# Kernel tuning notes

Hardware: AMD Instinct MI355X
Metric: run time of the kernel (lower is better)

Reference implementation:

```python
import jax, jax.numpy as jnp
import numpy as np

N_NODES = 100000
N_EDGES = 1600000
N_GRAPHS = 1024
D_IN = 128
D_HID = 128
D_OUT = 2


def setup_inputs() -> dict:
    key = jax.random.key(0)
    ks = jax.random.split(key, 12)
    x = jax.random.normal(ks[0], (N_NODES, D_IN), dtype=jnp.float32)
    edge_index = jax.random.randint(ks[1], (2, N_EDGES), 0, N_NODES, dtype=jnp.int32)
    batch = jnp.sort(jax.random.randint(ks[2], (N_NODES,), 0, N_GRAPHS, dtype=jnp.int32))
    def lin(k, fan_in, fan_out):
        bound = 1.0 / np.sqrt(fan_in)
        kw, kb = jax.random.split(k)
        W = jax.random.uniform(kw, (fan_in, fan_out), minval=-bound, maxval=bound, dtype=jnp.float32)
        b = jax.random.uniform(kb, (fan_out,), minval=-bound, maxval=bound, dtype=jnp.float32)
        return W, b
    W1, b1 = lin(ks[3], D_IN, D_HID)
    W2, b2 = lin(ks[4], D_HID, D_HID)
    fc1_w, fc1_b = lin(ks[5], D_HID, D_HID)
    fc2_w, fc2_b = lin(ks[6], D_HID, D_OUT)
    return {"x": x, "edge_index": edge_index, "batch": batch,
            "W1": W1, "b1": b1, "W2": W2, "b2": b2,
            "fc1_w": fc1_w, "fc1_b": fc1_b, "fc2_w": fc2_w, "fc2_b": fc2_b}


def gcn_conv(x, W, b, src, dst, deg_inv_sqrt, n_nodes):
    # GCNConv: out = D^-1/2 (A + I) D^-1/2 (x W) + b, using edge list with self-loops
    h = x @ W  # [N, d_out]
    norm = deg_inv_sqrt[src] * deg_inv_sqrt[dst]  # [E+N]
    msg = h[src] * norm[:, None]  # gather + scale
    out = jnp.zeros((n_nodes, h.shape[1]), dtype=h.dtype).at[dst].add(msg)
    return out + b


def reference(x, edge_index, batch, W1, b1, W2, b2, fc1_w, fc1_b, fc2_w, fc2_b):
    n = x.shape[0]
    loops = jnp.arange(n, dtype=edge_index.dtype)
    src = jnp.concatenate([edge_index[0], loops])  # add self-loops (PyG default)
    dst = jnp.concatenate([edge_index[1], loops])
    deg = jnp.zeros((n,), dtype=x.dtype).at[dst].add(1.0)
    deg_inv_sqrt = jax.lax.rsqrt(deg)  # deg >= 1 due to self-loops

    h = jax.nn.relu(gcn_conv(x, W1, b1, src, dst, deg_inv_sqrt, n))
    # dropout p=0.5 is identity in eval mode
    h = jax.nn.relu(gcn_conv(h, W2, b2, src, dst, deg_inv_sqrt, n))

    # global_mean_pool over batch assignment
    sums = jax.ops.segment_sum(h, batch, num_segments=N_GRAPHS)
    cnts = jax.ops.segment_sum(jnp.ones((n,), dtype=h.dtype), batch, num_segments=N_GRAPHS)
    pooled = sums / jnp.maximum(cnts, 1.0)[:, None]  # [G, d]

    g = jax.nn.relu(pooled @ fc1_w + fc1_b)
    logits = g @ fc2_w + fc2_b
    return jax.nn.log_softmax(logits, axis=1)
```

## Files before the change

### kernel.cpp

```cpp
#include <hip/hip_runtime.h>
#include <hip/hip_fp16.h>
#include <math.h>


#define D_FEAT 128
#define BSHIFT 9
#define BNODES 512
#define CHUNK 4096
#define CAPB 16384
#define PCAP 16384
#define CAP 10240

using half8   = __attribute__((ext_vector_type(8))) _Float16;
using half4   = __attribute__((ext_vector_type(4))) _Float16;
using floatx4 = __attribute__((ext_vector_type(4))) float;
using floatx2 = __attribute__((ext_vector_type(2))) float;

__global__ void __launch_bounds__(256) binA_kernel(const int* __restrict__ edges,
                                                   int* __restrict__ gcur,
                                                   int* __restrict__ binned, int E, int nb) {
    __shared__ int h[256];
    __shared__ int cur[256];
    __shared__ int base[256];
    int t = threadIdx.x;
    int c0 = blockIdx.x * CHUNK;
    int sv[CHUNK / 256], bv[CHUNK / 256];
    int i0 = c0 + t * (CHUNK / 256);
    if (i0 + (CHUNK / 256) <= E) {
#pragma unroll
        for (int k = 0; k < CHUNK / 256; k += 4) {
            int4 s4 = *(const int4*)&edges[i0 + k];
            int4 d4 = *(const int4*)&edges[E + i0 + k];
            bv[k + 0] = d4.x >> BSHIFT; sv[k + 0] = ((d4.x & (BNODES - 1)) << 17) | s4.x;
            bv[k + 1] = d4.y >> BSHIFT; sv[k + 1] = ((d4.y & (BNODES - 1)) << 17) | s4.y;
            bv[k + 2] = d4.z >> BSHIFT; sv[k + 2] = ((d4.z & (BNODES - 1)) << 17) | s4.z;
            bv[k + 3] = d4.w >> BSHIFT; sv[k + 3] = ((d4.w & (BNODES - 1)) << 17) | s4.w;
        }
    } else {
#pragma unroll
        for (int k = 0; k < CHUNK / 256; ++k) {
            int i = i0 + k;
            if (i < E) {
                int s = edges[i], d = edges[E + i];
                bv[k] = d >> BSHIFT;
                sv[k] = ((d & (BNODES - 1)) << 17) | s;
            } else bv[k] = -1;
        }
    }
    h[t] = 0;
    __syncthreads();
#pragma unroll
    for (int k = 0; k < CHUNK / 256; ++k)
        if (bv[k] >= 0) atomicAdd(&h[bv[k]], 1);
    __syncthreads();
    if (t < nb && h[t] > 0) base[t] = atomicAdd(&gcur[t], h[t]);
    cur[t] = 0;
    __syncthreads();
#pragma unroll
    for (int k = 0; k < CHUNK / 256; ++k)
        if (bv[k] >= 0) {
            int b = bv[k];
            int r = atomicAdd(&cur[b], 1);
            int pos = base[b] + r;
            if (pos < CAPB) binned[b * CAPB + pos] = sv[k];
        }
}

__global__ void __launch_bounds__(256) binB_kernel(const int* __restrict__ binned,
                                                   const int* __restrict__ gcur,
                                                   float* __restrict__ dis,
                                                   int* __restrict__ rowbeg,
                                                   int* __restrict__ rowend,
                                                   int* __restrict__ csr,
                                                   int N, int nb) {
    __shared__ int hist[BNODES];
    __shared__ int cur[BNODES];
    __shared__ int pend[BNODES];
    __shared__ int sdata[256];
    __shared__ int vals[CAP];
    int t = threadIdx.x;
    int b = blockIdx.x;
    int node0 = b << BSHIFT;
    int cnt = gcur[b];
    const int* bin = binned + (size_t)b * CAPB;
    hist[t] = 0; hist[t + 256] = 0;
    __syncthreads();
    for (int i = t; i < cnt; i += 256) {
        int v = bin[i];
        if (i < CAP) vals[i] = v;
        atomicAdd(&hist[v >> 17], 1);
    }
    __syncthreads();
    int a0 = hist[2 * t], a1 = hist[2 * t + 1];
    int p0sz = (a0 + 15) & ~15, p1sz = (a1 + 15) & ~15;
    int pair = p0sz + p1sz;
    sdata[t] = pair;
    __syncthreads();
    for (int d = 1; d < 256; d <<= 1) {
        int u = (t >= d) ? sdata[t - d] : 0;
        __syncthreads();
        sdata[t] += u;
        __syncthreads();
    }
    int excl = sdata[t] - pair;
    int q0 = b * PCAP + excl, q1 = q0 + p0sz;
    cur[2 * t] = q0;
    cur[2 * t + 1] = q1;
    pend[2 * t] = q1;
    pend[2 * t + 1] = q1 + p1sz;
    int n0 = node0 + 2 * t, n1 = node0 + 2 * t + 1;
    if (n0 < N) {
        rowbeg[n0] = q0; rowend[n0] = q1;
        dis[n0] = rsqrtf((float)a0 + 1.0f);
    }
    if (n1 < N) {
        rowbeg[n1] = q1; rowend[n1] = q1 + p1sz;
        dis[n1] = rsqrtf((float)a1 + 1.0f);
    }
    __syncthreads();
    for (int i = t; i < cnt; i += 256) {
        int v = (i < CAP) ? vals[i] : bin[i];
        int p = atomicAdd(&cur[v >> 17], 1);
        csr[p] = v & 0x1FFFF;
    }
    __syncthreads();
    for (int i = t; i < BNODES; i += 256) {
        int e = pend[i];
        for (int p = cur[i]; p < e; ++p) csr[p] = N;
    }
}

__global__ void wprep_kernel(const float* __restrict__ W1, const float* __restrict__ W2,
                             _Float16* __restrict__ Wt1, _Float16* __restrict__ Wt2,
                             unsigned int* __restrict__ zrow) {
    int i = blockIdx.x * blockDim.x + threadIdx.x;
    int n = i >> 7, k = i & 127;
    Wt1[i] = (_Float16)W1[k * 128 + n];
    Wt2[i] = (_Float16)W2[k * 128 + n];
    if (i < 32) zrow[i] = 0u;
}

template <bool HALF_IN>
__global__ void __launch_bounds__(256) gemm_mfma_kernel(const void* __restrict__ Xv,
                                                        const _Float16* __restrict__ WtG,
                                                        const float* __restrict__ dis,
                                                        unsigned char* __restrict__ Y8, int N) {
    __shared__ _Float16 wt[128][136];
    int t = threadIdx.x;
    int row0 = blockIdx.x * 64;

#pragma unroll
    for (int i = 0; i < 8; ++i) {
        int c = t + i * 256;
        int r = c >> 4, c8 = (c & 15) * 8;
        *(half8*)&wt[r][c8] = *(const half8*)&WtG[r * 128 + c8];
    }

    int wave = t >> 6, lane = t & 63;
    int m = lane & 15, quad = lane >> 4;
    int grow = row0 + wave * 16 + m;

    half8 a[4];
    if (grow < N) {
        if (HALF_IN) {
            const _Float16* Xp = (const _Float16*)Xv;
#pragma unroll
            for (int k = 0; k < 4; ++k)
                a[k] = *(const half8*)&Xp[(size_t)grow * 128 + k * 32 + quad * 8];
        } else {
            const float* Xp = (const float*)Xv;
#pragma unroll
            for (int k = 0; k < 4; ++k) {
                float4 v0 = *(const float4*)&Xp[(size_t)grow * 128 + k * 32 + quad * 8];
                float4 v1 = *(const float4*)&Xp[(size_t)grow * 128 + k * 32 + quad * 8 + 4];
                a[k] = (half8){(_Float16)v0.x, (_Float16)v0.y, (_Float16)v0.z, (_Float16)v0.w,
                               (_Float16)v1.x, (_Float16)v1.y, (_Float16)v1.z, (_Float16)v1.w};
            }
        }
    } else {
#pragma unroll
        for (int k = 0; k < 4; ++k) a[k] = (half8){};
    }
    __syncthreads();

    floatx4 acc[8];
#pragma unroll
    for (int nt = 0; nt < 8; ++nt) acc[nt] = (floatx4){0.f, 0.f, 0.f, 0.f};
#pragma unroll
    for (int nt = 0; nt < 8; ++nt) {
#pragma unroll
        for (int k = 0; k < 4; ++k) {
            half8 bfr = *(const half8*)&wt[nt * 16 + m][k * 32 + quad * 8];
            acc[nt] = __builtin_amdgcn_mfma_f32_16x16x32_f16(a[k], bfr, acc[nt], 0, 0, 0);
        }
    }
    int orow = row0 + wave * 16 + quad * 4;
#pragma unroll
    for (int r = 0; r < 4; ++r) {
        int row = orow + r;
        if (row < N) {
            float dr = dis[row];
#pragma unroll
            for (int nt = 0; nt < 8; ++nt) {
                float v = acc[nt][r] * dr;
                unsigned char q =
                    (unsigned char)(__builtin_amdgcn_cvt_pk_fp8_f32(v, v, 0, false) & 0xff);
                Y8[(size_t)row * 128 + nt * 16 + m] = q;
            }
        }
    }
}

__global__ void __launch_bounds__(256) agg_kernel(const unsigned char* __restrict__ H8,
                                                  const int* __restrict__ rowbeg,
                                                  const int* __restrict__ rowend,
                                                  const int* __restrict__ csr,
                                                  const float* __restrict__ dis,
                                                  const float* __restrict__ bias,
                                                  _Float16* __restrict__ out, int N) {
    int v = (blockIdx.x * blockDim.x + threadIdx.x) >> 6;
    int lane = threadIdx.x & 63;
    if (v >= N) return;
    int half = lane >> 5, sl = lane & 31;
    int r0 = rowbeg[v], r1 = rowend[v];
    float dv = dis[v];
    unsigned fo = (unsigned)(sl << 2);

    floatx2 a01, a23;
    {
        unsigned int u = *(const unsigned int*)(H8 + (((unsigned)v << 7) | fo));
        floatx2 lo = __builtin_amdgcn_cvt_pk_f32_fp8(u, false);
        floatx2 hi = __builtin_amdgcn_cvt_pk_f32_fp8(u, true);
        floatx2 hf = {0.5f, 0.5f};
        a01 = hf * lo;
        a23 = hf * hi;
    }
#define ACC(uu)                                                         \
        {                                                               \
            a01 += __builtin_amdgcn_cvt_pk_f32_fp8(uu, false);          \
            a23 += __builtin_amdgcn_cvt_pk_f32_fp8(uu, true);           \
        }
    for (int e = r0 + half; e + 14 < r1; e += 16) {
        int s0 = csr[e],      s1 = csr[e + 2],  s2 = csr[e + 4],  s3 = csr[e + 6];
        int s4 = csr[e + 8],  s5 = csr[e + 10], s6 = csr[e + 12], s7 = csr[e + 14];
        unsigned int u0 = *(const unsigned int*)(H8 + (((unsigned)s0 << 7) | fo));
        unsigned int u1 = *(const unsigned int*)(H8 + (((unsigned)s1 << 7) | fo));
        unsigned int u2 = *(const unsigned int*)(H8 + (((unsigned)s2 << 7) | fo));
        unsigned int u3 = *(const unsigned int*)(H8 + (((unsigned)s3 << 7) | fo));
        unsigned int u4 = *(const unsigned int*)(H8 + (((unsigned)s4 << 7) | fo));
        unsigned int u5 = *(const unsigned int*)(H8 + (((unsigned)s5 << 7) | fo));
        unsigned int u6 = *(const unsigned int*)(H8 + (((unsigned)s6 << 7) | fo));
        unsigned int u7 = *(const unsigned int*)(H8 + (((unsigned)s7 << 7) | fo));
        ACC(u0) ACC(u1) ACC(u2) ACC(u3) ACC(u4) ACC(u5) ACC(u6) ACC(u7)
    }
#undef ACC
    a01[0] += __shfl_xor(a01[0], 32, 64);
    a01[1] += __shfl_xor(a01[1], 32, 64);
    a23[0] += __shfl_xor(a23[0], 32, 64);
    a23[1] += __shfl_xor(a23[1], 32, 64);
    if (half == 0) {
        float4 b = *(const float4*)&bias[sl * 4];
        half4 o = {(_Float16)fmaxf(dv * a01[0] + b.x, 0.f),
                   (_Float16)fmaxf(dv * a01[1] + b.y, 0.f),
                   (_Float16)fmaxf(dv * a23[0] + b.z, 0.f),
                   (_Float16)fmaxf(dv * a23[1] + b.w, 0.f)};
        *(half4*)&out[(size_t)v * 128 + sl * 4] = o;
    }
}

__device__ __forceinline__ int lower_bound_i(const int* a, int n, int key) {
    int lo = 0, hi = n;
    while (lo < hi) {
        int mid = (lo + hi) >> 1;
        if (a[mid] < key) lo = mid + 1;
        else hi = mid;
    }
    return lo;
}

__global__ void __launch_bounds__(512) poolhead_kernel(const _Float16* __restrict__ H,
                                                       const int* __restrict__ batch,
                                                       const float* __restrict__ fc1w,
                                                       const float* __restrict__ fc1b,
                                                       const float* __restrict__ fc2w,
                                                       const float* __restrict__ fc2b,
                                                       float* __restrict__ out, int N) {
    __shared__ int range[2];
    __shared__ float part[4][128];
    __shared__ float p[128];
    __shared__ float r0s[128], r1s[128];
    int g = blockIdx.x;
    int t = threadIdx.x;
    int j = t & 127, rg = t >> 7;
    if (t < 2) range[t] = lower_bound_i(batch, N, g + t);
    __syncthreads();
    int lo = range[0], hi = range[1];
    float s = 0.f;
    for (int v = lo + rg; v < hi; v += 4) s += (float)H[(size_t)v * 128 + j];
    part[rg][j] = s;
    __syncthreads();
    if (rg == 0) {
        float tot = part[0][j] + part[1][j] + part[2][j] + part[3][j];
        p[j] = tot / fmaxf((float)(hi - lo), 1.0f);
    }
    __syncthreads();
    if (t < 128) {
        float acc = fc1b[t];
#pragma unroll 8
        for (int k = 0; k < 128; ++k) acc = fmaf(p[k], fc1w[k * 128 + t], acc);
        float gv = fmaxf(acc, 0.f);
        r0s[t] = gv * fc2w[t * 2 + 0];
        r1s[t] = gv * fc2w[t * 2 + 1];
    }
    __syncthreads();
    for (int st = 64; st > 0; st >>= 1) {
        if (t < st) {
            r0s[t] += r0s[t + st];
            r1s[t] += r1s[t + st];
        }
        __syncthreads();
    }
    if (t == 0) {
        float l0 = r0s[0] + fc2b[0];
        float l1 = r1s[0] + fc2b[1];
        float m = fmaxf(l0, l1);
        float lse = m + logf(expf(l0 - m) + expf(l1 - m));
        out[g * 2 + 0] = l0 - lse;
        out[g * 2 + 1] = l1 - lse;
    }
}

extern "C" void kernel_launch(void* const* d_in, const int* in_sizes, int n_in,
                              void* d_out, int out_size, void* d_ws, size_t ws_size,
                              hipStream_t stream) {
    const float* x    = (const float*)d_in[0];
    const int* edges  = (const int*)d_in[1];
    const int* batch  = (const int*)d_in[2];
    const float* W1   = (const float*)d_in[3];
    const float* b1   = (const float*)d_in[4];
    const float* W2   = (const float*)d_in[5];
    const float* b2   = (const float*)d_in[6];
    const float* fc1w = (const float*)d_in[7];
    const float* fc1b = (const float*)d_in[8];
    const float* fc2w = (const float*)d_in[9];
    const float* fc2b = (const float*)d_in[10];
    float* out = (float*)d_out;

    int N = in_sizes[2];
    int E = in_sizes[1] / 2;
    int G = out_size / 2;
    int nb = (N + BNODES - 1) / BNODES;
    int nA = (E + CHUNK - 1) / CHUNK;

    char* ws = (char*)d_ws;
    size_t off = 0;
    auto alloc = [&](size_t bytes) -> char* {
        char* ptr = ws + off;
        off += (bytes + 255) & ~(size_t)255;
        return ptr;
    };
    int* gcur          = (int*)alloc((size_t)nb * 4);
    int* binned        = (int*)alloc((size_t)nb * CAPB * 4);
    int* rowbeg        = (int*)alloc((size_t)N * 4);
    int* rowend        = (int*)alloc((size_t)N * 4);
    float* dis         = (float*)alloc((size_t)N * 4);
    int* csr           = (int*)alloc((size_t)nb * PCAP * 4);
    _Float16* Wt1      = (_Float16*)alloc(128 * 128 * 2);
    _Float16* Wt2      = (_Float16*)alloc(128 * 128 * 2);
    unsigned char* buf8 = (unsigned char*)alloc((size_t)(N + 1) * D_FEAT);
    _Float16* bufH     = (_Float16*)alloc((size_t)N * D_FEAT * 2);

    hipMemsetAsync(gcur, 0, (size_t)nb * 4, stream);

    binA_kernel<<<nA, 256, 0, stream>>>(edges, gcur, binned, E, nb);
    binB_kernel<<<nb, 256, 0, stream>>>(binned, gcur, dis, rowbeg, rowend, csr, N, nb);
    wprep_kernel<<<64, 256, 0, stream>>>(W1, W2, Wt1, Wt2,
                                         (unsigned int*)(buf8 + (size_t)N * D_FEAT));

    int gAgg = (N * 64 + 255) / 256;
    int gGemm = (N + 63) / 64;
    gemm_mfma_kernel<false><<<gGemm, 256, 0, stream>>>((const void*)x, Wt1, dis, buf8, N);
    agg_kernel<<<gAgg, 256, 0, stream>>>(buf8, rowbeg, rowend, csr, dis, b1, bufH, N);
    gemm_mfma_kernel<true><<<gGemm, 256, 0, stream>>>((const void*)bufH, Wt2, dis, buf8, N);
    agg_kernel<<<gAgg, 256, 0, stream>>>(buf8, rowbeg, rowend, csr, dis, b2, bufH, N);
    poolhead_kernel<<<G, 512, 0, stream>>>(bufH, batch, fc1w, fc1b, fc2w, fc2b, out, N);
}
```

Before: 266.7 us.

## Fuse layer-1 aggregation with layer-2 GEMM into a single kernel

Replaces the first aggregation kernel plus the second GEMM with one kernel. Each block aggregates 16 nodes into an fp16 shared-memory tile, then runs MFMA against Wt2 and writes the dis-scaled fp8 output to a second buffer. This removes the fp16 round trip of the hidden features through global memory and one kernel launch. In exchange, each wave reads its Wt2 slice from global memory instead of shared memory, and the edge loop only handles full groups of 16 edges (rows are padded with zero-row indices).

```diff
diff --git a/kernel.cpp b/kernel.cpp
--- a/kernel.cpp
+++ b/kernel.cpp
@@ -132,12 +132,13 @@
 
 __global__ void wprep_kernel(const float* __restrict__ W1, const float* __restrict__ W2,
                              _Float16* __restrict__ Wt1, _Float16* __restrict__ Wt2,
-                             unsigned int* __restrict__ zrow) {
+                             unsigned int* __restrict__ zrow,
+                             unsigned int* __restrict__ zrow2) {
     int i = blockIdx.x * blockDim.x + threadIdx.x;
     int n = i >> 7, k = i & 127;
     Wt1[i] = (_Float16)W1[k * 128 + n];
     Wt2[i] = (_Float16)W2[k * 128 + n];
-    if (i < 32) zrow[i] = 0u;
+    if (i < 32) { zrow[i] = 0u; zrow2[i] = 0u; }
 }
 
 template <bool HALF_IN>
@@ -206,6 +207,104 @@
                 unsigned char q =
                     (unsigned char)(__builtin_amdgcn_cvt_pk_fp8_f32(v, v, 0, false) & 0xff);
                 Y8[(size_t)row * 128 + nt * 16 + m] = q;
+            }
+        }
+    }
+}
+
+__global__ void __launch_bounds__(256) fusedA_kernel(const unsigned char* __restrict__ H8,
+                                                     const int* __restrict__ rowbeg,
+                                                     const int* __restrict__ rowend,
+                                                     const int* __restrict__ csr,
+                                                     const float* __restrict__ dis,
+                                                     const float* __restrict__ bias,
+                                                     const _Float16* __restrict__ Wt2,
+                                                     unsigned char* __restrict__ Y8, int N) {
+    __shared__ _Float16 hl[16][136];
+    int t = threadIdx.x;
+    int wave = t >> 6, lane = t & 63;
+    int half = lane >> 5, sl = lane & 31;
+    unsigned fo = (unsigned)(sl << 2);
+    int vbase = blockIdx.x * 16 + wave * 4;
+
+#pragma unroll
+    for (int i = 0; i < 4; ++i) {
+        int v = vbase + i;
+        floatx2 a01 = {0.f, 0.f}, a23 = {0.f, 0.f};
+        float dv = 0.f;
+        if (v < N) {
+            int r0 = rowbeg[v], r1 = rowend[v];
+            dv = dis[v];
+            {
+                unsigned int u = *(const unsigned int*)(H8 + (((unsigned)v << 7) | fo));
+                floatx2 lo = __builtin_amdgcn_cvt_pk_f32_fp8(u, false);
+                floatx2 hi = __builtin_amdgcn_cvt_pk_f32_fp8(u, true);
+                floatx2 hf = {0.5f, 0.5f};
+                a01 = hf * lo;
+                a23 = hf * hi;
+            }
+#define ACC(uu)                                                         \
+            {                                                           \
+                a01 += __builtin_amdgcn_cvt_pk_f32_fp8(uu, false);      \
+                a23 += __builtin_amdgcn_cvt_pk_f32_fp8(uu, true);       \
+            }
+            for (int e = r0 + half; e + 14 < r1; e += 16) {
+                int s0 = csr[e],      s1 = csr[e + 2],  s2 = csr[e + 4],  s3 = csr[e + 6];
+                int s4 = csr[e + 8],  s5 = csr[e + 10], s6 = csr[e + 12], s7 = csr[e + 14];
+                unsigned int u0 = *(const unsigned int*)(H8 + (((unsigned)s0 << 7) | fo));
+                unsigned int u1 = *(const unsigned int*)(H8 + (((unsigned)s1 << 7) | fo));
+                unsigned int u2 = *(const unsigned int*)(H8 + (((unsigned)s2 << 7) | fo));
+                unsigned int u3 = *(const unsigned int*)(H8 + (((unsigned)s3 << 7) | fo));
+                unsigned int u4 = *(const unsigned int*)(H8 + (((unsigned)s4 << 7) | fo));
+                unsigned int u5 = *(const unsigned int*)(H8 + (((unsigned)s5 << 7) | fo));
+                unsigned int u6 = *(const unsigned int*)(H8 + (((unsigned)s6 << 7) | fo));
+                unsigned int u7 = *(const unsigned int*)(H8 + (((unsigned)s7 << 7) | fo));
+                ACC(u0) ACC(u1) ACC(u2) ACC(u3) ACC(u4) ACC(u5) ACC(u6) ACC(u7)
+            }
+#undef ACC
+        }
+        a01[0] += __shfl_xor(a01[0], 32, 64);
+        a01[1] += __shfl_xor(a01[1], 32, 64);
+        a23[0] += __shfl_xor(a23[0], 32, 64);
+        a23[1] += __shfl_xor(a23[1], 32, 64);
+        if (half == 0) {
+            float4 b = *(const float4*)&bias[sl * 4];
+            half4 o = {(_Float16)fmaxf(dv * a01[0] + b.x, 0.f),
+                       (_Float16)fmaxf(dv * a01[1] + b.y, 0.f),
+                       (_Float16)fmaxf(dv * a23[0] + b.z, 0.f),
+                       (_Float16)fmaxf(dv * a23[1] + b.w, 0.f)};
+            *(half4*)&hl[wave * 4 + i][sl * 4] = o;
+        }
+    }
+    __syncthreads();
+
+    int m = lane & 15, quad = lane >> 4;
+    half8 a[4];
+#pragma unroll
+    for (int k = 0; k < 4; ++k) a[k] = *(const half8*)&hl[m][k * 32 + quad * 8];
+    floatx4 acc[2];
+    acc[0] = (floatx4){0.f, 0.f, 0.f, 0.f};
+    acc[1] = (floatx4){0.f, 0.f, 0.f, 0.f};
+    int nt0 = wave * 2;
+#pragma unroll
+    for (int j = 0; j < 2; ++j)
+#pragma unroll
+        for (int k = 0; k < 4; ++k) {
+            half8 bfr = *(const half8*)&Wt2[(size_t)((nt0 + j) * 16 + m) * 128 + k * 32 + quad * 8];
+            acc[j] = __builtin_amdgcn_mfma_f32_16x16x32_f16(a[k], bfr, acc[j], 0, 0, 0);
+        }
+    int orow = blockIdx.x * 16 + quad * 4;
+#pragma unroll
+    for (int r = 0; r < 4; ++r) {
+        int row = orow + r;
+        if (row < N) {
+            float dr = dis[row];
+#pragma unroll
+            for (int j = 0; j < 2; ++j) {
+                float vv = acc[j][r] * dr;
+                unsigned char q =
+                    (unsigned char)(__builtin_amdgcn_cvt_pk_fp8_f32(vv, vv, 0, false) & 0xff);
+                Y8[(size_t)row * 128 + (nt0 + j) * 16 + m] = q;
             }
         }
     }
@@ -367,7 +466,8 @@
     int* csr           = (int*)alloc((size_t)nb * PCAP * 4);
     _Float16* Wt1      = (_Float16*)alloc(128 * 128 * 2);
     _Float16* Wt2      = (_Float16*)alloc(128 * 128 * 2);
-    unsigned char* buf8 = (unsigned char*)alloc((size_t)(N + 1) * D_FEAT);
+    unsigned char* buf8  = (unsigned char*)alloc((size_t)(N + 1) * D_FEAT);
+    unsigned char* buf8b = (unsigned char*)alloc((size_t)(N + 1) * D_FEAT);
     _Float16* bufH     = (_Float16*)alloc((size_t)N * D_FEAT * 2);
 
     hipMemsetAsync(gcur, 0, (size_t)nb * 4, stream);
@@ -375,13 +475,15 @@
     binA_kernel<<<nA, 256, 0, stream>>>(edges, gcur, binned, E, nb);
     binB_kernel<<<nb, 256, 0, stream>>>(binned, gcur, dis, rowbeg, rowend, csr, N, nb);
     wprep_kernel<<<64, 256, 0, stream>>>(W1, W2, Wt1, Wt2,
-                                         (unsigned int*)(buf8 + (size_t)N * D_FEAT));
+                                         (unsigned int*)(buf8 + (size_t)N * D_FEAT),
+                                         (unsigned int*)(buf8b + (size_t)N * D_FEAT));
 
     int gAgg = (N * 64 + 255) / 256;
     int gGemm = (N + 63) / 64;
+    int gFused = (N + 15) / 16;
     gemm_mfma_kernel<false><<<gGemm, 256, 0, stream>>>((const void*)x, Wt1, dis, buf8, N);
-    agg_kernel<<<gAgg, 256, 0, stream>>>(buf8, rowbeg, rowend, csr, dis, b1, bufH, N);
-    gemm_mfma_kernel<true><<<gGemm, 256, 0, stream>>>((const void*)bufH, Wt2, dis, buf8, N);
-    agg_kernel<<<gAgg, 256, 0, stream>>>(buf8, rowbeg, rowend, csr, dis, b2, bufH, N);
+    fusedA_kernel<<<gFused, 256, 0, stream>>>(buf8, rowbeg, rowend, csr, dis, b1, Wt2,
+                                              buf8b, N);
+    agg_kernel<<<gAgg, 256, 0, stream>>>(buf8b, rowbeg, rowend, csr, dis, b2, bufH, N);
     poolhead_kernel<<<G, 512, 0, stream>>>(bufH, batch, fc1w, fc1b, fc2w, fc2b, out, N);
 }
```

Measured after the change: 277.3 us. 4.0% more time.

## Build CSR with global atomic degree count, scan and scatter

Applied to the files above, without the earlier changes.

Replaces the two-stage binned CSR build with three kernels. The old scheme did a shared-memory histogram plus a bin append, then a per-bin local sort. The new scheme counts per-node degrees with global atomics, computes padded row offsets per 512-node block, and scatters source indices into CSR slots through global atomic cursors. It drops the large intermediate binned buffer and its extra read/write pass, but it reads the edge list twice and relies on many contended, scattered global atomics and uncoalesced writes.

```diff
diff --git a/kernel.cpp b/kernel.cpp
--- a/kernel.cpp
+++ b/kernel.cpp
@@ -6,92 +6,40 @@
 #define D_FEAT 128
 #define BSHIFT 9
 #define BNODES 512
-#define CHUNK 4096
-#define CAPB 16384
 #define PCAP 16384
-#define CAP 10240
 
 using half8   = __attribute__((ext_vector_type(8))) _Float16;
 using half4   = __attribute__((ext_vector_type(4))) _Float16;
 using floatx4 = __attribute__((ext_vector_type(4))) float;
 using floatx2 = __attribute__((ext_vector_type(2))) float;
 
-__global__ void __launch_bounds__(256) binA_kernel(const int* __restrict__ edges,
-                                                   int* __restrict__ gcur,
-                                                   int* __restrict__ binned, int E, int nb) {
-    __shared__ int h[256];
-    __shared__ int cur[256];
-    __shared__ int base[256];
-    int t = threadIdx.x;
-    int c0 = blockIdx.x * CHUNK;
-    int sv[CHUNK / 256], bv[CHUNK / 256];
-    int i0 = c0 + t * (CHUNK / 256);
-    if (i0 + (CHUNK / 256) <= E) {
-#pragma unroll
-        for (int k = 0; k < CHUNK / 256; k += 4) {
-            int4 s4 = *(const int4*)&edges[i0 + k];
-            int4 d4 = *(const int4*)&edges[E + i0 + k];
-            bv[k + 0] = d4.x >> BSHIFT; sv[k + 0] = ((d4.x & (BNODES - 1)) << 17) | s4.x;
-            bv[k + 1] = d4.y >> BSHIFT; sv[k + 1] = ((d4.y & (BNODES - 1)) << 17) | s4.y;
-            bv[k + 2] = d4.z >> BSHIFT; sv[k + 2] = ((d4.z & (BNODES - 1)) << 17) | s4.z;
-            bv[k + 3] = d4.w >> BSHIFT; sv[k + 3] = ((d4.w & (BNODES - 1)) << 17) | s4.w;
-        }
+__global__ void __launch_bounds__(256) deg_kernel(const int* __restrict__ edges,
+                                                  int* __restrict__ deg, int E) {
+    int i = (blockIdx.x * 256 + threadIdx.x) * 4;
+    if (i + 3 < E) {
+        int4 d4 = *(const int4*)&edges[E + i];
+        atomicAdd(&deg[d4.x], 1);
+        atomicAdd(&deg[d4.y], 1);
+        atomicAdd(&deg[d4.z], 1);
+        atomicAdd(&deg[d4.w], 1);
     } else {
-#pragma unroll
-        for (int k = 0; k < CHUNK / 256; ++k) {
-            int i = i0 + k;
-            if (i < E) {
-                int s = edges[i], d = edges[E + i];
-                bv[k] = d >> BSHIFT;
-                sv[k] = ((d & (BNODES - 1)) << 17) | s;
-            } else bv[k] = -1;
-        }
-    }
-    h[t] = 0;
-    __syncthreads();
-#pragma unroll
-    for (int k = 0; k < CHUNK / 256; ++k)
-        if (bv[k] >= 0) atomicAdd(&h[bv[k]], 1);
-    __syncthreads();
-    if (t < nb && h[t] > 0) base[t] = atomicAdd(&gcur[t], h[t]);
-    cur[t] = 0;
-    __syncthreads();
-#pragma unroll
-    for (int k = 0; k < CHUNK / 256; ++k)
-        if (bv[k] >= 0) {
-            int b = bv[k];
-            int r = atomicAdd(&cur[b], 1);
-            int pos = base[b] + r;
-            if (pos < CAPB) binned[b * CAPB + pos] = sv[k];
-        }
-}
-
-__global__ void __launch_bounds__(256) binB_kernel(const int* __restrict__ binned,
-                                                   const int* __restrict__ gcur,
+        for (; i < E; ++i) atomicAdd(&deg[edges[E + i]], 1);
+    }
+}
+
+__global__ void __launch_bounds__(256) scan_kernel(const int* __restrict__ deg,
                                                    float* __restrict__ dis,
                                                    int* __restrict__ rowbeg,
                                                    int* __restrict__ rowend,
-                                                   int* __restrict__ csr,
-                                                   int N, int nb) {
-    __shared__ int hist[BNODES];
-    __shared__ int cur[BNODES];
-    __shared__ int pend[BNODES];
+                                                   int* __restrict__ cur,
+                                                   int* __restrict__ csr, int N) {
     __shared__ int sdata[256];
-    __shared__ int vals[CAP];
     int t = threadIdx.x;
     int b = blockIdx.x;
     int node0 = b << BSHIFT;
-    int cnt = gcur[b];
-    const int* bin = binned + (size_t)b * CAPB;
-    hist[t] = 0; hist[t + 256] = 0;
-    __syncthreads();
-    for (int i = t; i < cnt; i += 256) {
-        int v = bin[i];
-        if (i < CAP) vals[i] = v;
-        atomicAdd(&hist[v >> 17], 1);
-    }
-    __syncthreads();
-    int a0 = hist[2 * t], a1 = hist[2 * t + 1];
+    int n0 = node0 + 2 * t, n1 = node0 + 2 * t + 1;
+    int a0 = (n0 < N) ? deg[n0] : 0;
+    int a1 = (n1 < N) ? deg[n1] : 0;
     int p0sz = (a0 + 15) & ~15, p1sz = (a1 + 15) & ~15;
     int pair = p0sz + p1sz;
     sdata[t] = pair;
@@ -104,29 +52,31 @@
     }
     int excl = sdata[t] - pair;
     int q0 = b * PCAP + excl, q1 = q0 + p0sz;
-    cur[2 * t] = q0;
-    cur[2 * t + 1] = q1;
-    pend[2 * t] = q1;
-    pend[2 * t + 1] = q1 + p1sz;
-    int n0 = node0 + 2 * t, n1 = node0 + 2 * t + 1;
     if (n0 < N) {
-        rowbeg[n0] = q0; rowend[n0] = q1;
+        rowbeg[n0] = q0; rowend[n0] = q1; cur[n0] = q0;
         dis[n0] = rsqrtf((float)a0 + 1.0f);
+        for (int p = q0 + a0; p < q1; ++p) csr[p] = N;
     }
     if (n1 < N) {
-        rowbeg[n1] = q1; rowend[n1] = q1 + p1sz;
+        rowbeg[n1] = q1; rowend[n1] = q1 + p1sz; cur[n1] = q1;
         dis[n1] = rsqrtf((float)a1 + 1.0f);
-    }
-    __syncthreads();
-    for (int i = t; i < cnt; i += 256) {
-        int v = (i < CAP) ? vals[i] : bin[i];
-        int p = atomicAdd(&cur[v >> 17], 1);
-        csr[p] = v & 0x1FFFF;
-    }
-    __syncthreads();
-    for (int i = t; i < BNODES; i += 256) {
-        int e = pend[i];
-        for (int p = cur[i]; p < e; ++p) csr[p] = N;
+        for (int p = q1 + a1; p < q1 + p1sz; ++p) csr[p] = N;
+    }
+}
+
+__global__ void __launch_bounds__(256) scat_kernel(const int* __restrict__ edges,
+                                                   int* __restrict__ cur,
+                                                   int* __restrict__ csr, int E) {
+    int i = (blockIdx.x * 256 + threadIdx.x) * 4;
+    if (i + 3 < E) {
+        int4 s4 = *(const int4*)&edges[i];
+        int4 d4 = *(const int4*)&edges[E + i];
+        csr[atomicAdd(&cur[d4.x], 1)] = s4.x;
+        csr[atomicAdd(&cur[d4.y], 1)] = s4.y;
+        csr[atomicAdd(&cur[d4.z], 1)] = s4.z;
+        csr[atomicAdd(&cur[d4.w], 1)] = s4.w;
+    } else {
+        for (; i < E; ++i) csr[atomicAdd(&cur[edges[E + i]], 1)] = edges[i];
     }
 }
 
@@ -350,7 +300,6 @@
     int E = in_sizes[1] / 2;
     int G = out_size / 2;
     int nb = (N + BNODES - 1) / BNODES;
-    int nA = (E + CHUNK - 1) / CHUNK;
 
     char* ws = (char*)d_ws;
     size_t off = 0;
@@ -359,8 +308,8 @@
         off += (bytes + 255) & ~(size_t)255;
         return ptr;
     };
-    int* gcur          = (int*)alloc((size_t)nb * 4);
-    int* binned        = (int*)alloc((size_t)nb * CAPB * 4);
+    int* deg           = (int*)alloc((size_t)N * 4);
+    int* cur           = (int*)alloc((size_t)N * 4);
     int* rowbeg        = (int*)alloc((size_t)N * 4);
     int* rowend        = (int*)alloc((size_t)N * 4);
     float* dis         = (float*)alloc((size_t)N * 4);
@@ -370,10 +319,12 @@
     unsigned char* buf8 = (unsigned char*)alloc((size_t)(N + 1) * D_FEAT);
     _Float16* bufH     = (_Float16*)alloc((size_t)N * D_FEAT * 2);
 
-    hipMemsetAsync(gcur, 0, (size_t)nb * 4, stream);
-
-    binA_kernel<<<nA, 256, 0, stream>>>(edges, gcur, binned, E, nb);
-    binB_kernel<<<nb, 256, 0, stream>>>(binned, gcur, dis, rowbeg, rowend, csr, N, nb);
+    hipMemsetAsync(deg, 0, (size_t)N * 4, stream);
+
+    int gE4 = (E / 4 + 255) / 256;
+    deg_kernel<<<gE4, 256, 0, stream>>>(edges, deg, E);
+    scan_kernel<<<nb, 256, 0, stream>>>(deg, dis, rowbeg, rowend, cur, csr, N);
+    scat_kernel<<<gE4, 256, 0, stream>>>(edges, cur, csr, E);
     wprep_kernel<<<64, 256, 0, stream>>>(W1, W2, Wt1, Wt2,
                                          (unsigned int*)(buf8 + (size_t)N * D_FEAT));
 
```

Result: slower. 411.9 us (+54.5%).

## Pack row metadata into int4 and prefetch CSR indices as vector loads in aggregation

Applied to the files above, without the earlier changes.

Row begin, end and degree-normalisation are packed into one int4 per node, so each aggregation wave does one 16-byte metadata load instead of three scalar loads. Neighbour indices are read as four int4 vector loads per 16 edges and software-prefetched one iteration ahead, so index fetch latency overlaps the feature gathers. Aggregation blocks shrink from 256 to 128 threads. This relies on row segments being 16-aligned and padded, which binB already guarantees, and adds register pressure for the prefetch buffers.

```diff
diff --git a/kernel.cpp b/kernel.cpp
--- a/kernel.cpp
+++ b/kernel.cpp
@@ -69,8 +69,7 @@
 __global__ void __launch_bounds__(256) binB_kernel(const int* __restrict__ binned,
                                                    const int* __restrict__ gcur,
                                                    float* __restrict__ dis,
-                                                   int* __restrict__ rowbeg,
-                                                   int* __restrict__ rowend,
+                                                   int4* __restrict__ rowext,
                                                    int* __restrict__ csr,
                                                    int N, int nb) {
     __shared__ int hist[BNODES];
@@ -110,12 +109,14 @@
     pend[2 * t + 1] = q1 + p1sz;
     int n0 = node0 + 2 * t, n1 = node0 + 2 * t + 1;
     if (n0 < N) {
-        rowbeg[n0] = q0; rowend[n0] = q1;
-        dis[n0] = rsqrtf((float)a0 + 1.0f);
+        float d0 = rsqrtf((float)a0 + 1.0f);
+        dis[n0] = d0;
+        rowext[n0] = (int4){q0, q1, __float_as_int(d0), 0};
     }
     if (n1 < N) {
-        rowbeg[n1] = q1; rowend[n1] = q1 + p1sz;
-        dis[n1] = rsqrtf((float)a1 + 1.0f);
+        float d1 = rsqrtf((float)a1 + 1.0f);
+        dis[n1] = d1;
+        rowext[n1] = (int4){q1, q1 + p1sz, __float_as_int(d1), 0};
     }
     __syncthreads();
     for (int i = t; i < cnt; i += 256) {
@@ -211,19 +212,18 @@
     }
 }
 
-__global__ void __launch_bounds__(256) agg_kernel(const unsigned char* __restrict__ H8,
-                                                  const int* __restrict__ rowbeg,
-                                                  const int* __restrict__ rowend,
+__global__ void __launch_bounds__(128) agg_kernel(const unsigned char* __restrict__ H8,
+                                                  const int4* __restrict__ rowext,
                                                   const int* __restrict__ csr,
-                                                  const float* __restrict__ dis,
                                                   const float* __restrict__ bias,
                                                   _Float16* __restrict__ out, int N) {
-    int v = (blockIdx.x * blockDim.x + threadIdx.x) >> 6;
+    int v = (blockIdx.x * 128 + threadIdx.x) >> 6;
     int lane = threadIdx.x & 63;
     if (v >= N) return;
     int half = lane >> 5, sl = lane & 31;
-    int r0 = rowbeg[v], r1 = rowend[v];
-    float dv = dis[v];
+    int4 re = rowext[v];
+    int r0 = re.x, len = re.y - re.x;
+    float dv = __int_as_float(re.z);
     unsigned fo = (unsigned)(sl << 2);
 
     floatx2 a01, a23;
@@ -235,14 +235,24 @@
         a01 = hf * lo;
         a23 = hf * hi;
     }
+    const int4* cp = (const int4*)(csr + r0);
+    int4 cb0, cb1, cb2, cb3;
+    if (len > 0) { cb0 = cp[0]; cb1 = cp[1]; cb2 = cp[2]; cb3 = cp[3]; }
 #define ACC(uu)                                                         \
         {                                                               \
             a01 += __builtin_amdgcn_cvt_pk_f32_fp8(uu, false);          \
             a23 += __builtin_amdgcn_cvt_pk_f32_fp8(uu, true);           \
         }
-    for (int e = r0 + half; e + 14 < r1; e += 16) {
-        int s0 = csr[e],      s1 = csr[e + 2],  s2 = csr[e + 4],  s3 = csr[e + 6];
-        int s4 = csr[e + 8],  s5 = csr[e + 10], s6 = csr[e + 12], s7 = csr[e + 14];
+    for (int base = 0; base < len; base += 16) {
+        int4 c0 = cb0, c1 = cb1, c2 = cb2, c3 = cb3;
+        if (base + 16 < len) {
+            const int4* np = cp + ((base >> 4) + 1) * 4;
+            cb0 = np[0]; cb1 = np[1]; cb2 = np[2]; cb3 = np[3];
+        }
+        int s0 = half ? c0.y : c0.x,  s1 = half ? c0.w : c0.z;
+        int s2 = half ? c1.y : c1.x,  s3 = half ? c1.w : c1.z;
+        int s4 = half ? c2.y : c2.x,  s5 = half ? c2.w : c2.z;
+        int s6 = half ? c3.y : c3.x,  s7 = half ? c3.w : c3.z;
         unsigned int u0 = *(const unsigned int*)(H8 + (((unsigned)s0 << 7) | fo));
         unsigned int u1 = *(const unsigned int*)(H8 + (((unsigned)s1 << 7) | fo));
         unsigned int u2 = *(const unsigned int*)(H8 + (((unsigned)s2 << 7) | fo));
@@ -361,8 +371,7 @@
     };
     int* gcur          = (int*)alloc((size_t)nb * 4);
     int* binned        = (int*)alloc((size_t)nb * CAPB * 4);
-    int* rowbeg        = (int*)alloc((size_t)N * 4);
-    int* rowend        = (int*)alloc((size_t)N * 4);
+    int4* rowext       = (int4*)alloc((size_t)N * 16);
     float* dis         = (float*)alloc((size_t)N * 4);
     int* csr           = (int*)alloc((size_t)nb * PCAP * 4);
     _Float16* Wt1      = (_Float16*)alloc(128 * 128 * 2);
@@ -373,15 +382,15 @@
     hipMemsetAsync(gcur, 0, (size_t)nb * 4, stream);
 
     binA_kernel<<<nA, 256, 0, stream>>>(edges, gcur, binned, E, nb);
-    binB_kernel<<<nb, 256, 0, stream>>>(binned, gcur, dis, rowbeg, rowend, csr, N, nb);
+    binB_kernel<<<nb, 256, 0, stream>>>(binned, gcur, dis, rowext, csr, N, nb);
     wprep_kernel<<<64, 256, 0, stream>>>(W1, W2, Wt1, Wt2,
                                          (unsigned int*)(buf8 + (size_t)N * D_FEAT));
 
-    int gAgg = (N * 64 + 255) / 256;
+    int gAgg = (N + 1) / 2;
     int gGemm = (N + 63) / 64;
     gemm_mfma_kernel<false><<<gGemm, 256, 0, stream>>>((const void*)x, Wt1, dis, buf8, N);
-    agg_kernel<<<gAgg, 256, 0, stream>>>(buf8, rowbeg, rowend, csr, dis, b1, bufH, N);
+    agg_kernel<<<gAgg, 128, 0, stream>>>(buf8, rowext, csr, b1, bufH, N);
     gemm_mfma_kernel<true><<<gGemm, 256, 0, stream>>>((const void*)bufH, Wt2, dis, buf8, N);
-    agg_kernel<<<gAgg, 256, 0, stream>>>(buf8, rowbeg, rowend, csr, dis, b2, bufH, N);
+    agg_kernel<<<gAgg, 128, 0, stream>>>(buf8, rowext, csr, b2, bufH, N);
     poolhead_kernel<<<G, 512, 0, stream>>>(bufH, batch, fc1w, fc1b, fc2w, fc2b, out, N);
 }
```

Result: no change. 268.0 us (+0.5%).
